# Kernel tuning notes

Measured on AMD Instinct MI355X. Metric: run time of the kernel, lower is better.

## Reference

```python
import jax, jax.numpy as jnp
import numpy as np

T = 5  # frames per clip, hardcoded in the module
H = 8  # heads


def _to_heads(z, b, n_, h, dh):
    # '(b t) n (h d) -> b h (n t) d' with t=T
    z = z.reshape(b, T, n_, h, dh)
    z = z.transpose(0, 3, 2, 1, 4)  # b h n t d
    return z.reshape(b, h, n_ * T, dh)


def _from_heads(z, b, n_, h, dh):
    # 'b h (n t) d -> (b t) n (h d)'
    z = z.reshape(b, h, n_, T, dh)
    z = z.transpose(0, 3, 2, 1, 4)  # b t n h d
    return z.reshape(b * T, n_, h * dh)


def setup_inputs() -> dict:
    key = jax.random.key(0)
    ks = jax.random.split(key, 6)
    bt, n, dim = 160, 257, 512
    inner = 512
    x = jax.random.normal(ks[0], (bt, n, dim), dtype=jnp.float32)
    mask = jax.random.uniform(ks[1], (bt, 16, 16), dtype=jnp.float32)
    Wv_qkv = jax.random.normal(ks[2], (dim, inner * 3), dtype=jnp.float32) * (dim ** -0.5)
    Wa_qkv = jax.random.normal(ks[3], (dim, inner * 3), dtype=jnp.float32) * (dim ** -0.5)
    Wo = jax.random.normal(ks[4], (inner, dim), dtype=jnp.float32) * (inner ** -0.5)
    bo = jnp.zeros((dim,), dtype=jnp.float32)
    return {"x": x, "mask": mask, "Wv_qkv": Wv_qkv, "Wa_qkv": Wa_qkv, "Wo": Wo, "bo": bo}


def reference(x, mask, Wv_qkv, Wa_qkv, Wo, bo):
    bt, n, dim = x.shape
    b = bt // T
    h = H
    inner = Wv_qkv.shape[1] // 3
    dh = inner // h
    scale = dh ** -0.5

    A = x[:, :1]   # (bt, 1, dim)
    V = x[:, 1:]   # (bt, n-1, dim)

    v_qkv = jnp.split(V @ Wv_qkv, 3, axis=-1)
    a_qkv = jnp.split(A @ Wa_qkv, 3, axis=-1)
    qv, kv, vv = (_to_heads(z, b, n - 1, h, dh) for z in v_qkv)  # (b,h,(n-1)*T,dh)
    qa, ka, va = (_to_heads(z, b, 1, h, dh) for z in a_qkv)       # (b,h,T,dh)

    # multiplicative query mask: (bt,16,16) -> (bt, n-1, 1) broadcast to dim -> heads layout
    m = jnp.broadcast_to(mask.reshape(bt, n - 1, 1), (bt, n - 1, h * dh))
    m = _to_heads(m, b, n - 1, h, dh)
    qv = qv * m

    # audio queries attend over visual keys/values
    av_dots = jnp.einsum('bhqd,bhkd->bhqk', qa, kv) * scale  # (b,h,T,(n-1)*T)
    av_out = jnp.einsum('bhqk,bhkd->bhqd', jax.nn.softmax(av_dots, axis=-1), vv)

    # visual queries attend over audio keys/values
    va_dots = jnp.einsum('bhqd,bhkd->bhqk', qv, ka) * scale  # (b,h,(n-1)*T,T)
    va_out = jnp.einsum('bhqk,bhkd->bhqd', jax.nn.softmax(va_dots, axis=-1), va)

    a_out = _from_heads(av_out, b, 1, h, dh)      # (bt, 1, inner)
    v_out = _from_heads(va_out, b, n - 1, h, dh)  # (bt, n-1, inner)
    out = jnp.concatenate((a_out, v_out), axis=1)  # (bt, n, inner)
    return out @ Wo + bo
```

## Files before the change

### kernel.cpp

```cpp
#include <hip/hip_runtime.h>
#include <hip/hip_bf16.h>

typedef unsigned short u16;
typedef __bf16 bf16x8 __attribute__((ext_vector_type(8)));
typedef u16 u16x8 __attribute__((ext_vector_type(8)));
typedef float f32x4 __attribute__((ext_vector_type(4)));

__device__ __forceinline__ float bf2f(u16 u) {
    return __uint_as_float(((unsigned)u) << 16);
}
__device__ __forceinline__ u16 f2bf(float f) {
    unsigned u = __float_as_uint(f);
    unsigned r = (u + 0x7fffu + ((u >> 16) & 1u)) >> 16;
    return (u16)r;
}

__device__ __forceinline__ void gl_lds16(const u16* g, u16* l) {
    __builtin_amdgcn_global_load_lds(
        (const __attribute__((address_space(1))) void*)g,
        (__attribute__((address_space(3))) void*)l, 16, 0, 0);
}

__global__ __launch_bounds__(256) void prep(const float* __restrict__ x,
                                            const float* __restrict__ Wv,
                                            const float* __restrict__ Wa,
                                            const float* __restrict__ Wo,
                                            u16* __restrict__ xb,
                                            u16* __restrict__ WvTv,
                                            u16* __restrict__ WaT,
                                            u16* __restrict__ WoT) {
    __shared__ float tile[64][65];
    int blk = blockIdx.x;
    if (blk < 10280) {
        int i = (blk * 256 + threadIdx.x) * 8;
        float4 a = *(const float4*)&x[i];
        float4 b = *(const float4*)&x[i + 4];
        u16x8 o;
        o[0] = f2bf(a.x); o[1] = f2bf(a.y); o[2] = f2bf(a.z); o[3] = f2bf(a.w);
        o[4] = f2bf(b.x); o[5] = f2bf(b.y); o[6] = f2bf(b.z); o[7] = f2bf(b.w);
        *(u16x8*)&xb[i] = o;
        return;
    }
    blk -= 10280;
    const float* W; u16* WT; int N, stride, coff;
    if (blk < 64)       { W = Wv; WT = WvTv; N = 512;  stride = 1536; coff = 1024; }
    else if (blk < 256) { W = Wa; WT = WaT;  N = 1536; stride = 1536; coff = 0; blk -= 64; }
    else                { W = Wo; WT = WoT;  N = 512;  stride = 512;  coff = 0; blk -= 256; }
    const int nt = N >> 6;
    const int k0 = (blk / nt) << 6;
    const int n0 = (blk % nt) << 6;
    for (int i = threadIdx.x; i < 4096; i += 256) {
        int r = i >> 6, c = i & 63;
        tile[r][c] = W[(size_t)(k0 + r) * stride + coff + n0 + c];
    }
    __syncthreads();
    for (int i = threadIdx.x; i < 4096; i += 256) {
        int r = i >> 6, c = i & 63;
        WT[(size_t)(n0 + r) * 512 + k0 + c] = f2bf(tile[c][r]);
    }
}

template <int MODE, int OUTF>
__global__ __launch_bounds__(256) void gemm_k(const u16* __restrict__ A,
                                              const u16* __restrict__ Bt,
                                              void* __restrict__ Cv,
                                              const float* __restrict__ bias,
                                              int M, int N, int K) {
    __shared__ u16 As[128][64];
    __shared__ u16 Bs[128][64];
    const int t = threadIdx.x;
    const int bn0 = blockIdx.x * 128;
    const int bm0 = blockIdx.y * 128;
    const int wave = t >> 6, lane = t & 63;
    const int wm = (wave >> 1) * 64, wn = (wave & 1) * 64;
    const int lr = lane & 15, lh = lane >> 4;
    const int srow = wave * 8 + (lane >> 3);
    const int scol = (lane & 7) * 8;

    f32x4 acc[4][4] = {};

    for (int kt = 0; kt < K; kt += 64) {
        __syncthreads();
#pragma unroll
        for (int i = 0; i < 4; i++) {
            int row = i * 32 + srow;
            int r = bm0 + row;
            long g;
            if (MODE == 0) g = (r < M) ? (long)r : 0l;
            else           g = (r < M) ? (long)r * 257 : 0l;
            gl_lds16(&A[g * K + kt + scol], &As[0][0] + i * 2048 + wave * 512);
            long nr = bn0 + row;
            gl_lds16(&Bt[nr * K + kt + scol], &Bs[0][0] + i * 2048 + wave * 512);
        }
        __syncthreads();
#pragma unroll
        for (int kk = 0; kk < 2; kk++) {
            bf16x8 af[4], bfr[4];
#pragma unroll
            for (int mi = 0; mi < 4; mi++)
                af[mi] = *(const bf16x8*)&As[wm + mi * 16 + lr][kk * 32 + lh * 8];
#pragma unroll
            for (int ni = 0; ni < 4; ni++)
                bfr[ni] = *(const bf16x8*)&Bs[wn + ni * 16 + lr][kk * 32 + lh * 8];
#pragma unroll
            for (int mi = 0; mi < 4; mi++)
#pragma unroll
                for (int ni = 0; ni < 4; ni++)
                    acc[mi][ni] = __builtin_amdgcn_mfma_f32_16x16x32_bf16(
                        af[mi], bfr[ni], acc[mi][ni], 0, 0, 0);
        }
    }

#pragma unroll
    for (int mi = 0; mi < 4; mi++)
#pragma unroll
        for (int ni = 0; ni < 4; ni++)
#pragma unroll
            for (int r2 = 0; r2 < 4; r2++) {
                int m = bm0 + wm + mi * 16 + lh * 4 + r2;
                if (m < M) {
                    int nc = bn0 + wn + ni * 16 + lr;
                    float v = acc[mi][ni][r2];
                    if (OUTF == 2) ((float*)Cv)[(size_t)m * 257 * N + nc] = v + bias[nc];
                    else           ((u16*)Cv)[(size_t)m * N + nc] = f2bf(v);
                }
            }
}

__global__ __launch_bounds__(1024) void gemm_vs(const u16* __restrict__ A,
                                                const u16* __restrict__ WvTv,
                                                const u16* __restrict__ wcomb,
                                                u16* __restrict__ vv,
                                                float* __restrict__ pglob,
                                                float* __restrict__ vascore) {
    __shared__ u16 As[2][256][64];
    __shared__ u16 Bs[2][256][64];
    const int t = threadIdx.x;
    const int nwg = gridDim.x;
    const int orig = blockIdx.x;
    const int qc = nwg >> 3;
    const int xcd = orig & 7, slot = orig >> 3;
    const int wgid = xcd * qc + slot;
    const int my = wgid / 3, sec = wgid % 3;
    const int bm0 = my * 256;
    const int bt = my, b = bt / 5, t5 = bt - b * 5;
    const int bn0 = (sec < 2) ? sec * 256 : 0;
    const u16* Bt = (sec < 2) ? WvTv : (wcomb + (size_t)b * 256 * 512);
    const int wave = t >> 6, lane = t & 63;
    const int wm = (wave >> 2) * 64, wn = (wave & 3) * 64;
    const int lr = lane & 15, lh = lane >> 4;
    const int xr = (lr & 7) << 3;
    u16* AsF = &As[0][0][0];
    u16* BsF = &Bs[0][0][0];

    const int gsa = ((lane & 7) ^ (lane >> 3)) * 8;
    auto stage = [&](int buf, int kt_) {
        const int kc = kt_ * 64;
#pragma unroll
        for (int j = 0; j < 2; j++) {
            int c0 = j * 1024 + wave * 64;
            int row = (c0 + lane) >> 3;
            int r = bm0 + row;
            long ga = (long)(r >> 8) * 257 + (r & 255) + 1;
            gl_lds16(&A[ga * 512 + kc + gsa], AsF + buf * 16384 + c0 * 8);
            gl_lds16(&Bt[(long)(bn0 + row) * 512 + kc + gsa], BsF + buf * 16384 + c0 * 8);
        }
    };

    f32x4 acc[4][4] = {};

    stage(0, 0);
    __builtin_amdgcn_sched_barrier(0);
    asm volatile("s_waitcnt vmcnt(0)" ::: "memory");
    __builtin_amdgcn_s_barrier();
    __builtin_amdgcn_sched_barrier(0);

    int cur = 0;
    for (int kt = 0; kt < 8; kt++) {
        if (kt + 1 < 8) {
            stage(cur ^ 1, kt + 1);
            __builtin_amdgcn_sched_barrier(0);
        }
        __builtin_amdgcn_s_setprio(1);
#pragma unroll
        for (int kk = 0; kk < 2; kk++) {
            bf16x8 af[4], bfr[4];
#pragma unroll
            for (int mi = 0; mi < 4; mi++)
                af[mi] = *(const bf16x8*)&As[cur][wm + mi * 16 + lr][(kk * 32 + lh * 8) ^ xr];
#pragma unroll
            for (int ni = 0; ni < 4; ni++)
                bfr[ni] = *(const bf16x8*)&Bs[cur][wn + ni * 16 + lr][(kk * 32 + lh * 8) ^ xr];
#pragma unroll
            for (int mi = 0; mi < 4; mi++)
#pragma unroll
                for (int ni = 0; ni < 4; ni++)
                    acc[mi][ni] = __builtin_amdgcn_mfma_f32_16x16x32_bf16(
                        af[mi], bfr[ni], acc[mi][ni], 0, 0, 0);
        }
        __builtin_amdgcn_s_setprio(0);
        if (kt == 7) break;
        __builtin_amdgcn_sched_barrier(0);
        asm volatile("s_waitcnt vmcnt(0)" ::: "memory");
        __builtin_amdgcn_s_barrier();
        __builtin_amdgcn_sched_barrier(0);
        cur ^= 1;
    }

    if (sec < 2) {
#pragma unroll
        for (int mi = 0; mi < 4; mi++)
#pragma unroll
            for (int ni = 0; ni < 4; ni++)
#pragma unroll
                for (int r2 = 0; r2 < 4; r2++) {
                    int m = bm0 + wm + mi * 16 + lh * 4 + r2;
                    int nc = bn0 + wn + ni * 16 + lr;
                    vv[(size_t)m * 512 + nc] = f2bf(acc[mi][ni][r2]);
                }
    } else {
#pragma unroll
        for (int ni = 0; ni < 4; ni++) {
            const int c = wn + ni * 16 + lr;
            if (c < 40) {
                const int h = c / 5, q = c - h * 5;
                float* prow = &pglob[((size_t)(b * 8 + h) * 5 + q) * 1280];
#pragma unroll
                for (int mi = 0; mi < 4; mi++)
#pragma unroll
                    for (int r2 = 0; r2 < 4; r2++) {
                        int m = bm0 + wm + mi * 16 + lh * 4 + r2;
                        int j = m & 255;
                        prow[j * 5 + t5] = acc[mi][ni][r2];
                    }
            } else if (c < 80) {
#pragma unroll
                for (int mi = 0; mi < 4; mi++)
#pragma unroll
                    for (int r2 = 0; r2 < 4; r2++) {
                        int m = bm0 + wm + mi * 16 + lh * 4 + r2;
                        vascore[(size_t)m * 40 + (c - 40)] = acc[mi][ni][r2];
                    }
            }
        }
    }
}

__global__ __launch_bounds__(512) void wbuild_all(const float* __restrict__ Wv,
                                                  const float* __restrict__ Wo,
                                                  const u16* __restrict__ aqkv,
                                                  u16* __restrict__ wcomb,
                                                  u16* __restrict__ vob) {
    const int blk = blockIdx.x;
    const int t = threadIdx.x;
    if (blk < 128) {
        __shared__ float avec[20][64];
        const int kind = blk & 1, h = (blk >> 1) & 7, vc = blk >> 4;
        const int v0 = vc * 20;
        const int aoff = (kind == 0) ? 0 : 512;
        for (int i = t; i < 1280; i += 512) {
            int vi = i >> 6, d = i & 63;
            int v = v0 + vi, b = v / 5, q = v - b * 5;
            avec[vi][d] = bf2f(aqkv[(size_t)(b * 5 + q) * 1536 + aoff + h * 64 + d]);
        }
        const int k = t;
        const int colbase = (kind == 0) ? (512 + h * 64) : (h * 64);
        float wr[64];
#pragma unroll
        for (int d = 0; d < 64; d += 4) {
            float4 w4 = *(const float4*)&Wv[(size_t)k * 1536 + colbase + d];
            wr[d] = w4.x; wr[d + 1] = w4.y; wr[d + 2] = w4.z; wr[d + 3] = w4.w;
        }
        __syncthreads();
        for (int vi = 0; vi < 20; vi++) {
            float acc = 0.f;
#pragma unroll
            for (int d = 0; d < 64; d++) acc += wr[d] * avec[vi][d];
            int v = v0 + vi, b = v / 5, q = v - b * 5;
            int c = kind * 40 + h * 5 + q;
            wcomb[((size_t)b * 256 + c) * 512 + k] = f2bf(acc);
        }
        return;
    }
    {
        __shared__ float vaL[5][64];
        const int bh = blk - 128;
        const int b = bh >> 3, h = bh & 7;
        for (int i = t; i < 320; i += 512) {
            int q = i >> 6, d = i & 63;
            vaL[q][d] = bf2f(aqkv[(size_t)(b * 5 + q) * 1536 + 1024 + h * 64 + d]);
        }
        __syncthreads();
        const int c = t;
        float a0 = 0, a1 = 0, a2 = 0, a3 = 0, a4 = 0;
#pragma unroll 8
        for (int d = 0; d < 64; d++) {
            float w = Wo[(size_t)(h * 64 + d) * 512 + c];
            a0 += w * vaL[0][d];
            a1 += w * vaL[1][d];
            a2 += w * vaL[2][d];
            a3 += w * vaL[3][d];
            a4 += w * vaL[4][d];
        }
        const size_t base = ((size_t)b * 512 + c) * 64;
        vob[base + h * 5]     = f2bf(a0);
        vob[base + h * 5 + 1] = f2bf(a1);
        vob[base + h * 5 + 2] = f2bf(a2);
        vob[base + h * 5 + 3] = f2bf(a3);
        vob[base + h * 5 + 4] = f2bf(a4);
        if (h == 0) {
#pragma unroll
            for (int i = 40; i < 64; i++) vob[base + i] = 0;
        }
    }
}

__global__ __launch_bounds__(256) void vaout(const float* __restrict__ vascore,
                                             const float* __restrict__ mask,
                                             const u16* __restrict__ vob,
                                             const float* __restrict__ bo,
                                             float* __restrict__ out) {
    __shared__ u16 As[128][64];
    __shared__ u16 Bs[128][64];
    const int blk = blockIdx.x;
    const int nh = blk & 3, mh = (blk >> 2) & 1, bt = blk >> 3;
    const int b = bt / 5;
    const int t = threadIdx.x;
    if (t < 128) {
        const int rr = mh * 128 + t;
        const size_t m = (size_t)bt * 256 + rr;
        const float mval = mask[m] * 0.125f;
        const float* sp = &vascore[m * 40];
        u16 prow[64];
#pragma unroll
        for (int h = 0; h < 8; h++) {
            float r0 = sp[h * 5] * mval, r1 = sp[h * 5 + 1] * mval, r2 = sp[h * 5 + 2] * mval;
            float r3 = sp[h * 5 + 3] * mval, r4 = sp[h * 5 + 4] * mval;
            float mx = fmaxf(fmaxf(fmaxf(r0, r1), fmaxf(r2, r3)), r4);
            float e0 = __expf(r0 - mx), e1 = __expf(r1 - mx), e2 = __expf(r2 - mx);
            float e3 = __expf(r3 - mx), e4 = __expf(r4 - mx);
            float inv = 1.f / (e0 + e1 + e2 + e3 + e4);
            prow[h * 5]     = f2bf(e0 * inv);
            prow[h * 5 + 1] = f2bf(e1 * inv);
            prow[h * 5 + 2] = f2bf(e2 * inv);
            prow[h * 5 + 3] = f2bf(e3 * inv);
            prow[h * 5 + 4] = f2bf(e4 * inv);
        }
#pragma unroll
        for (int i = 40; i < 64; i++) prow[i] = 0;
#pragma unroll
        for (int s = 0; s < 8; s++)
            *(u16x8*)&As[t][s * 8] = *(u16x8*)&prow[s * 8];
    }
    for (int i = t; i < 1024; i += 256) {
        int r = i >> 3, seg = i & 7;
        *(u16x8*)&Bs[r][seg * 8] =
            *(const u16x8*)&vob[((size_t)b * 512 + nh * 128 + r) * 64 + seg * 8];
    }
    __syncthreads();

    const int wave = t >> 6, lane = t & 63;
    const int wm = (wave >> 1) * 64, wn = (wave & 1) * 64;
    const int lr = lane & 15, lh = lane >> 4;
    f32x4 acc[4][4] = {};
#pragma unroll
    for (int kk = 0; kk < 2; kk++) {
        bf16x8 af[4], bfr[4];
#pragma unroll
        for (int mi = 0; mi < 4; mi++)
            af[mi] = *(const bf16x8*)&As[wm + mi * 16 + lr][kk * 32 + lh * 8];
#pragma unroll
        for (int ni = 0; ni < 4; ni++)
            bfr[ni] = *(const bf16x8*)&Bs[wn + ni * 16 + lr][kk * 32 + lh * 8];
#pragma unroll
        for (int mi = 0; mi < 4; mi++)
#pragma unroll
            for (int ni = 0; ni < 4; ni++)
                acc[mi][ni] = __builtin_amdgcn_mfma_f32_16x16x32_bf16(
                    af[mi], bfr[ni], acc[mi][ni], 0, 0, 0);
    }

    const size_t obase = ((size_t)bt * 257 + 1 + mh * 128) * 512 + nh * 128;
#pragma unroll
    for (int mi = 0; mi < 4; mi++)
#pragma unroll
        for (int ni = 0; ni < 4; ni++)
#pragma unroll
            for (int r2 = 0; r2 < 4; r2++) {
                int row = wm + mi * 16 + lh * 4 + r2;
                int col = wn + ni * 16 + lr;
                out[obase + (size_t)row * 512 + col] = acc[mi][ni][r2] + bo[nh * 128 + col];
            }
}

__global__ __launch_bounds__(1024) void av_finish(const u16* __restrict__ vv,
                                                  const float* __restrict__ pglob,
                                                  u16* __restrict__ catA) {
    __shared__ float pl[5][1280];
    __shared__ float pbuf[16][5][64];
    const int bh = blockIdx.x;
    const int bi = bh >> 3, hd = bh & 7;
    const int t = threadIdx.x;
    for (int i = t; i < 6400; i += 1024) {
        pl[0][i] = pglob[(size_t)bh * 6400 + i] * 0.125f;
    }
    __syncthreads();
    const int wave = t >> 6, lane = t & 63;
    if (wave < 5) {
        float v[20];
        float mx = -3.4e38f;
#pragma unroll
        for (int i = 0; i < 20; i++) {
            v[i] = pl[wave][lane + i * 64];
            mx = fmaxf(mx, v[i]);
        }
#pragma unroll
        for (int off = 32; off > 0; off >>= 1) mx = fmaxf(mx, __shfl_xor(mx, off));
        float sum = 0.f;
#pragma unroll
        for (int i = 0; i < 20; i++) {
            v[i] = __expf(v[i] - mx);
            sum += v[i];
        }
#pragma unroll
        for (int off = 32; off > 0; off >>= 1) sum += __shfl_xor(sum, off);
        const float inv = 1.f / sum;
#pragma unroll
        for (int i = 0; i < 20; i++) pl[wave][lane + i * 64] = v[i] * inv;
    }
    __syncthreads();
    {
        float a0 = 0, a1 = 0, a2 = 0, a3 = 0, a4 = 0;
        const int j0 = wave * 16;
        for (int jj = 0; jj < 16; jj++) {
            const int j = j0 + jj;
#pragma unroll
            for (int t5 = 0; t5 < 5; t5++) {
                float v = bf2f(vv[(size_t)((bi * 5 + t5) * 256 + j) * 512 + hd * 64 + lane]);
                const int s = j * 5 + t5;
                a0 += pl[0][s] * v;
                a1 += pl[1][s] * v;
                a2 += pl[2][s] * v;
                a3 += pl[3][s] * v;
                a4 += pl[4][s] * v;
            }
        }
        pbuf[wave][0][lane] = a0;
        pbuf[wave][1][lane] = a1;
        pbuf[wave][2][lane] = a2;
        pbuf[wave][3][lane] = a3;
        pbuf[wave][4][lane] = a4;
    }
    __syncthreads();
    if (t < 320) {
        const int q = t >> 6, d = t & 63;
        float s = 0.f;
#pragma unroll
        for (int w = 0; w < 16; w++) s += pbuf[w][q][d];
        catA[(size_t)(bi * 5 + q) * 512 + hd * 64 + d] = f2bf(s);
    }
}

extern "C" void kernel_launch(void* const* d_in, const int* in_sizes, int n_in,
                              void* d_out, int out_size, void* d_ws, size_t ws_size,
                              hipStream_t stream) {
    const float* x    = (const float*)d_in[0];
    const float* mask = (const float*)d_in[1];
    const float* Wv   = (const float*)d_in[2];
    const float* Wa   = (const float*)d_in[3];
    const float* Wo   = (const float*)d_in[4];
    const float* bo   = (const float*)d_in[5];
    float* out = (float*)d_out;

    char* ws = (char*)d_ws;
    u16*   xb      = (u16*)(ws);
    u16*   WvTv    = (u16*)(ws + 42106880);
    u16*   WaT     = (u16*)(ws + 42631168);
    u16*   WoT     = (u16*)(ws + 44204032);
    u16*   aqkv    = (u16*)(ws + 44728320);
    u16*   wcomb   = (u16*)(ws + 45219840);
    u16*   vv      = (u16*)(ws + 53608448);
    float* vascore = (float*)(ws + 95551488);
    float* pglob   = (float*)(ws + 102105088);
    u16*   catA    = (u16*)(ws + 108658688);
    u16*   vob     = (u16*)(ws + 109969408);

    prep<<<dim3(10600), 256, 0, stream>>>(x, Wv, Wa, Wo, xb, WvTv, WaT, WoT);

    gemm_k<2, 0><<<dim3(12, 2), 256, 0, stream>>>(xb, WaT, aqkv, nullptr, 160, 1536, 512);

    wbuild_all<<<dim3(384), 512, 0, stream>>>(Wv, Wo, aqkv, wcomb, vob);

    gemm_vs<<<dim3(480), 1024, 0, stream>>>(xb, WvTv, wcomb, vv, pglob, vascore);

    vaout<<<dim3(1280), 256, 0, stream>>>(vascore, mask, vob, bo, out);

    av_finish<<<dim3(256), 1024, 0, stream>>>(vv, pglob, catA);

    gemm_k<0, 2><<<dim3(4, 2), 256, 0, stream>>>(catA, WoT, out, bo, 160, 512, 512);
}
```

Before: 157.2 us.

## Merge vaout and av_finish into one heterogeneous attn_out kernel launch

Fuses the visual-query output kernel and the audio-query finishing kernel into a single launch, using the block index to pick which job a block runs (256 av blocks, 640 va blocks). Both now use 512-thread blocks; va blocks cover 256 rows instead of 128, and av blocks use 8 waves each handling 32 positions. The aim is to drop one kernel launch and let the two independent workloads run on the device at the same time. In exchange, per-block register and shared-memory use is set by the larger of the two paths, which may reduce occupancy.

```diff
diff --git a/kernel.cpp b/kernel.cpp
--- a/kernel.cpp
+++ b/kernel.cpp
@@ -315,19 +315,90 @@
     }
 }
 
-__global__ __launch_bounds__(256) void vaout(const float* __restrict__ vascore,
-                                             const float* __restrict__ mask,
-                                             const u16* __restrict__ vob,
-                                             const float* __restrict__ bo,
-                                             float* __restrict__ out) {
-    __shared__ u16 As[128][64];
-    __shared__ u16 Bs[128][64];
+__global__ __launch_bounds__(512) void attn_out(const u16* __restrict__ vv,
+                                                const float* __restrict__ pglob,
+                                                u16* __restrict__ catA,
+                                                const float* __restrict__ vascore,
+                                                const float* __restrict__ mask,
+                                                const u16* __restrict__ vob,
+                                                const float* __restrict__ bo,
+                                                float* __restrict__ out) {
+    __shared__ __align__(16) char shm[49152];
     const int blk = blockIdx.x;
-    const int nh = blk & 3, mh = (blk >> 2) & 1, bt = blk >> 3;
+    const int t = threadIdx.x;
+    const int wave = t >> 6, lane = t & 63;
+
+    if (blk < 256) {
+        float* pl   = (float*)shm;
+        float* pbuf = (float*)(shm + 25600);
+        const int bh = blk;
+        const int bi = bh >> 3, hd = bh & 7;
+        for (int i = t; i < 6400; i += 512)
+            pl[i] = pglob[(size_t)bh * 6400 + i] * 0.125f;
+        __syncthreads();
+        if (wave < 5) {
+            float v[20];
+            float mx = -3.4e38f;
+#pragma unroll
+            for (int i = 0; i < 20; i++) {
+                v[i] = pl[wave * 1280 + lane + i * 64];
+                mx = fmaxf(mx, v[i]);
+            }
+#pragma unroll
+            for (int off = 32; off > 0; off >>= 1) mx = fmaxf(mx, __shfl_xor(mx, off));
+            float sum = 0.f;
+#pragma unroll
+            for (int i = 0; i < 20; i++) {
+                v[i] = __expf(v[i] - mx);
+                sum += v[i];
+            }
+#pragma unroll
+            for (int off = 32; off > 0; off >>= 1) sum += __shfl_xor(sum, off);
+            const float inv = 1.f / sum;
+#pragma unroll
+            for (int i = 0; i < 20; i++) pl[wave * 1280 + lane + i * 64] = v[i] * inv;
+        }
+        __syncthreads();
+        {
+            float a0 = 0, a1 = 0, a2 = 0, a3 = 0, a4 = 0;
+            const int j0 = wave * 32;
+            for (int jj = 0; jj < 32; jj++) {
+                const int j = j0 + jj;
+#pragma unroll
+                for (int t5 = 0; t5 < 5; t5++) {
+                    float v = bf2f(vv[(size_t)((bi * 5 + t5) * 256 + j) * 512 + hd * 64 + lane]);
+                    const int s = j * 5 + t5;
+                    a0 += pl[0 * 1280 + s] * v;
+                    a1 += pl[1 * 1280 + s] * v;
+                    a2 += pl[2 * 1280 + s] * v;
+                    a3 += pl[3 * 1280 + s] * v;
+                    a4 += pl[4 * 1280 + s] * v;
+                }
+            }
+            pbuf[(wave * 5 + 0) * 64 + lane] = a0;
+            pbuf[(wave * 5 + 1) * 64 + lane] = a1;
+            pbuf[(wave * 5 + 2) * 64 + lane] = a2;
+            pbuf[(wave * 5 + 3) * 64 + lane] = a3;
+            pbuf[(wave * 5 + 4) * 64 + lane] = a4;
+        }
+        __syncthreads();
+        if (t < 320) {
+            const int q = t >> 6, d = t & 63;
+            float s = 0.f;
+#pragma unroll
+            for (int w = 0; w < 8; w++) s += pbuf[(w * 5 + q) * 64 + d];
+            catA[(size_t)(bi * 5 + q) * 512 + hd * 64 + d] = f2bf(s);
+        }
+        return;
+    }
+
+    const int blk2 = blk - 256;
+    const int nh = blk2 & 3, bt = blk2 >> 2;
     const int b = bt / 5;
-    const int t = threadIdx.x;
-    if (t < 128) {
-        const int rr = mh * 128 + t;
+    u16* As = (u16*)shm;
+    u16* Bs = (u16*)(shm + 32768);
+    if (t < 256) {
+        const int rr = t;
         const size_t m = (size_t)bt * 256 + rr;
         const float mval = mask[m] * 0.125f;
         const float* sp = &vascore[m * 40];
@@ -350,17 +421,16 @@
         for (int i = 40; i < 64; i++) prow[i] = 0;
 #pragma unroll
         for (int s = 0; s < 8; s++)
-            *(u16x8*)&As[t][s * 8] = *(u16x8*)&prow[s * 8];
-    }
-    for (int i = t; i < 1024; i += 256) {
+            *(u16x8*)&As[rr * 64 + s * 8] = *(u16x8*)&prow[s * 8];
+    }
+    for (int i = t; i < 1024; i += 512) {
         int r = i >> 3, seg = i & 7;
-        *(u16x8*)&Bs[r][seg * 8] =
+        *(u16x8*)&Bs[r * 64 + seg * 8] =
             *(const u16x8*)&vob[((size_t)b * 512 + nh * 128 + r) * 64 + seg * 8];
     }
     __syncthreads();
 
-    const int wave = t >> 6, lane = t & 63;
-    const int wm = (wave >> 1) * 64, wn = (wave & 1) * 64;
+    const int wm3 = (wave >> 1) * 64, wn3 = (wave & 1) * 64;
     const int lr = lane & 15, lh = lane >> 4;
     f32x4 acc[4][4] = {};
 #pragma unroll
@@ -368,10 +438,10 @@
         bf16x8 af[4], bfr[4];
 #pragma unroll
         for (int mi = 0; mi < 4; mi++)
-            af[mi] = *(const bf16x8*)&As[wm + mi * 16 + lr][kk * 32 + lh * 8];
+            af[mi] = *(const bf16x8*)&As[(wm3 + mi * 16 + lr) * 64 + kk * 32 + lh * 8];
 #pragma unroll
         for (int ni = 0; ni < 4; ni++)
-            bfr[ni] = *(const bf16x8*)&Bs[wn + ni * 16 + lr][kk * 32 + lh * 8];
+            bfr[ni] = *(const bf16x8*)&Bs[(wn3 + ni * 16 + lr) * 64 + kk * 32 + lh * 8];
 #pragma unroll
         for (int mi = 0; mi < 4; mi++)
 #pragma unroll
@@ -380,85 +450,17 @@
                     af[mi], bfr[ni], acc[mi][ni], 0, 0, 0);
     }
 
-    const size_t obase = ((size_t)bt * 257 + 1 + mh * 128) * 512 + nh * 128;
+    const size_t obase = ((size_t)bt * 257 + 1) * 512 + nh * 128;
 #pragma unroll
     for (int mi = 0; mi < 4; mi++)
 #pragma unroll
         for (int ni = 0; ni < 4; ni++)
 #pragma unroll
             for (int r2 = 0; r2 < 4; r2++) {
-                int row = wm + mi * 16 + lh * 4 + r2;
-                int col = wn + ni * 16 + lr;
+                int row = wm3 + mi * 16 + lh * 4 + r2;
+                int col = wn3 + ni * 16 + lr;
                 out[obase + (size_t)row * 512 + col] = acc[mi][ni][r2] + bo[nh * 128 + col];
             }
-}
-
-__global__ __launch_bounds__(1024) void av_finish(const u16* __restrict__ vv,
-                                                  const float* __restrict__ pglob,
-                                                  u16* __restrict__ catA) {
-    __shared__ float pl[5][1280];
-    __shared__ float pbuf[16][5][64];
-    const int bh = blockIdx.x;
-    const int bi = bh >> 3, hd = bh & 7;
-    const int t = threadIdx.x;
-    for (int i = t; i < 6400; i += 1024) {
-        pl[0][i] = pglob[(size_t)bh * 6400 + i] * 0.125f;
-    }
-    __syncthreads();
-    const int wave = t >> 6, lane = t & 63;
-    if (wave < 5) {
-        float v[20];
-        float mx = -3.4e38f;
-#pragma unroll
-        for (int i = 0; i < 20; i++) {
-            v[i] = pl[wave][lane + i * 64];
-            mx = fmaxf(mx, v[i]);
-        }
-#pragma unroll
-        for (int off = 32; off > 0; off >>= 1) mx = fmaxf(mx, __shfl_xor(mx, off));
-        float sum = 0.f;
-#pragma unroll
-        for (int i = 0; i < 20; i++) {
-            v[i] = __expf(v[i] - mx);
-            sum += v[i];
-        }
-#pragma unroll
-        for (int off = 32; off > 0; off >>= 1) sum += __shfl_xor(sum, off);
-        const float inv = 1.f / sum;
-#pragma unroll
-        for (int i = 0; i < 20; i++) pl[wave][lane + i * 64] = v[i] * inv;
-    }
-    __syncthreads();
-    {
-        float a0 = 0, a1 = 0, a2 = 0, a3 = 0, a4 = 0;
-        const int j0 = wave * 16;
-        for (int jj = 0; jj < 16; jj++) {
-            const int j = j0 + jj;
-#pragma unroll
-            for (int t5 = 0; t5 < 5; t5++) {
-                float v = bf2f(vv[(size_t)((bi * 5 + t5) * 256 + j) * 512 + hd * 64 + lane]);
-                const int s = j * 5 + t5;
-                a0 += pl[0][s] * v;
-                a1 += pl[1][s] * v;
-                a2 += pl[2][s] * v;
-                a3 += pl[3][s] * v;
-                a4 += pl[4][s] * v;
-            }
-        }
-        pbuf[wave][0][lane] = a0;
-        pbuf[wave][1][lane] = a1;
-        pbuf[wave][2][lane] = a2;
-        pbuf[wave][3][lane] = a3;
-        pbuf[wave][4][lane] = a4;
-    }
-    __syncthreads();
-    if (t < 320) {
-        const int q = t >> 6, d = t & 63;
-        float s = 0.f;
-#pragma unroll
-        for (int w = 0; w < 16; w++) s += pbuf[w][q][d];
-        catA[(size_t)(bi * 5 + q) * 512 + hd * 64 + d] = f2bf(s);
-    }
 }
 
 extern "C" void kernel_launch(void* const* d_in, const int* in_sizes, int n_in,
@@ -493,9 +495,7 @@
 
     gemm_vs<<<dim3(480), 1024, 0, stream>>>(xb, WvTv, wcomb, vv, pglob, vascore);
 
-    vaout<<<dim3(1280), 256, 0, stream>>>(vascore, mask, vob, bo, out);
-
-    av_finish<<<dim3(256), 1024, 0, stream>>>(vv, pglob, catA);
+    attn_out<<<dim3(896), 512, 0, stream>>>(vv, pglob, catA, vascore, mask, vob, bo, out);
 
     gemm_k<0, 2><<<dim3(4, 2), 256, 0, stream>>>(catA, WoT, out, bo, 160, 512, 512);
 }
```

After: 155.3 us, median of 2. No clear change (-1.2%).
